# Performance work log

Hardware: AMD Instinct MI355X
Metric: run time of the kernel (lower is better)

## Reference

```python
import jax, jax.numpy as jnp
import numpy as np
from jax.scipy.linalg import solve_triangular

B, S, H, D, L = 8, 256, 768, 128, 64


def setup_inputs() -> dict:
    key = jax.random.key(0)
    ks = jax.random.split(key, 14)
    f = lambda k, shp, s=1.0: (jax.random.normal(k, shp, dtype=jnp.float32) * s)
    return {
        'word_feat_mean': f(ks[0], (B, S, H)),
        'word_feat_div': f(ks[1], (B, S, H)),
        'sent_feat_mean': f(ks[2], (B, 1, H)),
        'sent_feat_div': f(ks[3], (B, 1, H)),
        'W1': f(ks[4], (H, D), 0.02), 'b1': f(ks[5], (D,), 0.02),
        'W2': f(ks[6], (H, D), 0.02), 'b2': f(ks[7], (D,), 0.02),
        'W3': f(ks[8], (H, D), 0.02), 'b3': f(ks[9], (D,), 0.02),
        'W4': f(ks[10], (H, D), 0.02), 'b4': f(ks[11], (D,), 0.02),
        'label_mean': f(ks[12], (L, D)),
        'label_div_vec': f(ks[13], (L, D)),
    }


def _jsd_rank1(mu_p, v_p, mu_q, v_q):
    """Symmetric Gaussian JSD (0.5*(KL12+KL21)) between N(mu_p, I+v_p v_p^T) (labels, [L,D])
    and N(mu_q, I+v_q v_q^T) (words, [B,S,D]) via Sherman-Morrison closed form -> [B,L,S].
    Same math as torch.distributions MVN KL with Sigma = I + vv^T."""
    d = mu_p.shape[-1]
    n_p = 1.0 + jnp.sum(v_p * v_p, -1)            # [L]   = det(I+vp vp^T)
    n_q = 1.0 + jnp.sum(v_q * v_q, -1)            # [B,S]
    dot = jnp.einsum('ld,bsd->bls', v_p, v_q)     # vp.vq
    # ||mu_q - mu_p||^2 expanded without materializing [B,L,S,D]
    d2 = (jnp.sum(mu_q * mu_q, -1)[:, None, :]
          - 2.0 * jnp.einsum('ld,bsd->bls', mu_p, mu_q)
          + jnp.sum(mu_p * mu_p, -1)[None, :, None])
    vq_delta = (jnp.einsum('bsd,bsd->bs', v_q, mu_q)[:, None, :]
                - jnp.einsum('ld,bsd->bls', mu_p, v_q))
    vp_delta = (jnp.einsum('ld,bsd->bls', v_p, mu_q)
                - jnp.sum(v_p * mu_p, -1)[None, :, None])
    n_p_b = n_p[None, :, None]
    n_q_b = n_q[:, None, :]
    maha_q = d2 - vq_delta ** 2 / n_q_b           # delta^T Sigma_q^{-1} delta
    maha_p = d2 - vp_delta ** 2 / n_p_b
    tr_pq = d + (n_p_b - 1.0) - ((n_q_b - 1.0) + dot ** 2) / n_q_b  # tr(Sq^{-1} Sp)
    tr_qp = d + (n_q_b - 1.0) - ((n_p_b - 1.0) + dot ** 2) / n_p_b
    kl_pq = 0.5 * (jnp.log(n_q_b) - jnp.log(n_p_b) - d + tr_pq + maha_q)
    kl_qp = 0.5 * (jnp.log(n_p_b) - jnp.log(n_q_b) - d + tr_qp + maha_p)
    return 0.5 * (kl_pq + kl_qp)


def _jsd_full(mu_p, S_p, mu_q, S_q):
    """Symmetric JSD between full-covariance Gaussians, Cholesky-based (like torch MVN KL).
    mu_*: [..., D], S_*: [..., D, D] -> [...]."""
    d = mu_p.shape[-1]
    L_p = jnp.linalg.cholesky(S_p)
    L_q = jnp.linalg.cholesky(S_q)
    logdet_p = 2.0 * jnp.sum(jnp.log(jnp.diagonal(L_p, axis1=-2, axis2=-1)), -1)
    logdet_q = 2.0 * jnp.sum(jnp.log(jnp.diagonal(L_q, axis1=-2, axis2=-1)), -1)
    delta = mu_q - mu_p

    def kl(La, Lb, logda, logdb):
        # KL(a||b) = 0.5*(logdet_b - logdet_a - d + tr(Sb^{-1}Sa) + delta^T Sb^{-1} delta)
        X = solve_triangular(Lb, La, lower=True)
        tr = jnp.sum(X * X, axis=(-1, -2))
        y = solve_triangular(Lb, delta[..., None], lower=True)[..., 0]
        maha = jnp.sum(y * y, -1)
        return 0.5 * (logdb - logda - d + tr + maha)

    return 0.5 * (kl(L_p, L_q, logdet_p, logdet_q) + kl(L_q, L_p, logdet_q, logdet_p))


def reference(word_feat_mean, word_feat_div, sent_feat_mean, sent_feat_div,
              W1, b1, W2, b2, W3, b3, W4, b4, label_mean, label_div_vec):
    Bx, Sx, _ = word_feat_mean.shape
    Dx = W1.shape[1]
    Lx = label_mean.shape[0]
    wm = word_feat_mean @ W1 + b1        # jw1: [B,S,D]
    wv = word_feat_div @ W2 + b2         # jw2: [B,S,D]
    sm = sent_feat_mean @ W3 + b3        # jw3: [B,1,D]
    sv = sent_feat_div @ W4 + b4         # jw4: [B,1,D]
    eye = jnp.eye(Dx, dtype=wm.dtype)
    # Gaussian JSD attention: q = labels, k = v = words (closed-form, no [B,L*S,D,D])
    score = jax.nn.softmax(_jsd_rank1(label_mean, label_div_vec, wm, wv), axis=-1)  # [B,L,S]
    v_mean = jnp.einsum('bls,bsd->bld', score, wm)
    word_cov = eye + wv[..., :, None] * wv[..., None, :]                 # [B,S,D,D]
    v_div = jnp.einsum('bls,bsde->blde', score, word_cov)                # [B,L,D,D]
    sent_cov = eye + sv[..., :, None] * sv[..., None, :]                 # [B,1,D,D]
    text_mean = (sm + v_mean) / 2                                        # [B,L,D]
    text_div = (sent_cov + v_div) / 2                                    # [B,L,D,D]
    label_cov = eye + label_div_vec[:, :, None] * label_div_vec[:, None, :]  # [L,D,D]
    lm_b = jnp.broadcast_to(label_mean, (Bx, Lx, Dx))
    lc_b = jnp.broadcast_to(label_cov, (Bx, Lx, Dx, Dx))
    relate_score = _jsd_full(text_mean, text_div, lm_b, lc_b)            # [B,L]
    return relate_score, lm_b, lc_b
```

## Files before the change

kernel.cpp:

```cpp
#include <hip/hip_runtime.h>
#include <hip/hip_bf16.h>


#define PITCH 132

typedef __attribute__((ext_vector_type(8))) short bf16x8;
typedef __attribute__((ext_vector_type(4))) float f32x4;

__device__ __forceinline__ float bf2f(unsigned int u) {
    union { unsigned int i; float f; } c; c.i = u << 16; return c.f;
}
__device__ __forceinline__ unsigned short f2bf(float f) {
    __hip_bfloat16 h = __float2bfloat16(f);
    union { __hip_bfloat16 h; unsigned short u; } c; c.h = h; return c.u;
}

__global__ __launch_bounds__(256, 2)
void k1_gemm(const float* __restrict__ Am, const float* __restrict__ Av,
             const float* __restrict__ sfm, const float* __restrict__ sfd,
             const float* __restrict__ W1, const float* __restrict__ B1,
             const float* __restrict__ W2, const float* __restrict__ B2,
             const float* __restrict__ W3, const float* __restrict__ B3,
             const float* __restrict__ W4, const float* __restrict__ B4,
             float* __restrict__ wm, float* __restrict__ wv,
             float* __restrict__ sm, float* __restrict__ sv,
             unsigned short* __restrict__ wvTg) {
    __shared__ float At[16][64];
// ... 40 lines not shown
#pragma unroll
        for (int c = 0; c < 8; ++c) {
            float vl = acc[c] + Bs[j0 + c];
            D[ob + c] = vl;
            tileT[r][j0 + c] = vl;
        }
    }
    if (sel && !sentB) {
        __syncthreads();
        int d = tid >> 1, h = tid & 1;
        unsigned short u[8];
#pragma unroll
        for (int ss = 0; ss < 8; ++ss) u[ss] = f2bf(tileT[h * 8 + ss][d]);
        unsigned int p0 = (unsigned int)u[0] | ((unsigned int)u[1] << 16);
        unsigned int p1 = (unsigned int)u[2] | ((unsigned int)u[3] << 16);
        unsigned int p2 = (unsigned int)u[4] | ((unsigned int)u[5] << 16);
        unsigned int p3 = (unsigned int)u[6] | ((unsigned int)u[7] << 16);
        unsigned short* dst = wvTg + (size_t)(R0 >> 8) * 32768 + (size_t)d * 256 + (R0 & 255) + h * 8;
        *(uint4*)dst = make_uint4(p0, p1, p2, p3);
    }
}

template <int N>
__device__ __forceinline__ void bsumN(float* v, float* red) {
#pragma unroll
    for (int o = 32; o; o >>= 1)
#pragma unroll
        for (int n = 0; n < N; ++n) v[n] += __shfl_xor(v[n], o);
    __syncthreads();
    if ((threadIdx.x & 63) == 0) {
        int w = threadIdx.x >> 6;
#pragma unroll
        for (int n = 0; n < N; ++n) red[w * N + n] = v[n];
    }
    __syncthreads();
#pragma unroll
    for (int n = 0; n < N; ++n)
        v[n] = red[0 * N + n] + red[1 * N + n] + red[2 * N + n] + red[3 * N + n];
    __syncthreads();
}

__global__ __launch_bounds__(256, 2)
void k4_fused(const float* __restrict__ wm, const float* __restrict__ wv,
              const unsigned short* __restrict__ wvTg,
              const float* __restrict__ smg, const float* __restrict__ svg,
              const float* __restrict__ lmg, const float* __restrict__ ldvg,
              float* __restrict__ out) {
    extern __shared__ float smem[];
    float* Amat = smem;
    float* Wb   = smem + 16896;
    float* Sbuf = Wb;
    float* ssq  = smem + 19008;
    float* svr  = smem + 19264;
    float* vrow = smem + 19392;
    float* zv   = smem + 19520;
    float* zd   = smem + 19648;
    float* red  = smem + 19776;
    float* scoreL = Amat;
    float* vpart  = Amat + 256;

    const int tid = threadIdx.x;
    const int bid = blockIdx.x;
    const int b = bid >> 6, l = bid & 63;

    if (tid < 128) {
        svr[tid]  = svg[b * 128 + tid];
        vrow[tid] = ldvg[l * 128 + tid];
        zv[tid]   = lmg[l * 128 + tid];
    }
    __syncthreads();
    if (tid < 32) {
        float4 v = *(const float4*)&lmg[l * 128 + tid * 4];
        *(float4*)&out[512 + (size_t)bid * 128 + tid * 4] = v;
    }
    {
        float* lcb = out + 512 + 65536 + (size_t)bid * 16384;
#pragma unroll
        for (int q = 0; q < 16; ++q) {
            int flat4 = q * 256 + tid;
            int i = flat4 >> 5;
            int j4 = (flat4 & 31) * 4;
            float vi = vrow[i];
            float4 r;
            r.x = vi * vrow[j4 + 0] + ((i == j4 + 0) ? 1.f : 0.f);
            r.y = vi * vrow[j4 + 1] + ((i == j4 + 1) ? 1.f : 0.f);
            r.z = vi * vrow[j4 + 2] + ((i == j4 + 2) ? 1.f : 0.f);
            r.w = vi * vrow[j4 + 3] + ((i == j4 + 3) ? 1.f : 0.f);
            *(float4*)&lcb[(size_t)flat4 * 4] = r;
        }
    }
    float lv[3] = {0.f, 0.f, 0.f};
    if (tid < 128) {
        float m = zv[tid], v = vrow[tid];
        lv[0] = m * m; lv[1] = v * v; lv[2] = m * v;
    }
    bsumN<3>(lv, red);
    const float mmp = lv[0], np = 1.f + lv[1], vmp = lv[2];
    const float4* wmr = (const float4*)(wm + (size_t)(b * 256 + tid) * 128);
    const float4* wvr = (const float4*)(wv + (size_t)(b * 256 + tid) * 128);
    float md = 0.f, dot = 0.f, pvv = 0.f, vq = 0.f;
    float smm = 0.f, svv = 0.f, smv = 0.f;
#pragma unroll 8
    for (int q = 0; q < 32; ++q) {
        float4 xm = wmr[q], xv = wvr[q];
        const float* m4 = &zv[q * 4];
        const float* v4 = &vrow[q * 4];
        md  += m4[0] * xm.x + m4[1] * xm.y + m4[2] * xm.z + m4[3] * xm.w;
        dot += v4[0] * xv.x + v4[1] * xv.y + v4[2] * xv.z + v4[3] * xv.w;
        pvv += m4[0] * xv.x + m4[1] * xv.y + m4[2] * xv.z + m4[3] * xv.w;
        vq  += v4[0] * xm.x + v4[1] * xm.y + v4[2] * xm.z + v4[3] * xm.w;
        smm += xm.x * xm.x + xm.y * xm.y + xm.z * xm.z + xm.w * xm.w;
        svv += xv.x * xv.x + xv.y * xv.y + xv.z * xv.z + xv.w * xv.w;
        smv += xm.x * xv.x + xm.y * xv.y + xm.z * xv.z + xm.w * xv.w;
    }
    float nq = 1.f + svv;
    float d2 = smm - 2.f * md + mmp;
    float vqd = smv - pvv, vpd = vq - vmp;
    float inq = 1.f / nq, inp = 1.f / np;
    float maha_q = d2 - vqd * vqd * inq;
    float maha_p = d2 - vpd * vpd * inp;
    float logit = 0.25f * ((np - 1.f) + (nq - 1.f)
                           - (nq - 1.f + dot * dot) * inq
                           - (np - 1.f + dot * dot) * inp
                           + maha_q + maha_p);
    float mx = logit;
#pragma unroll
    for (int o = 32; o; o >>= 1) mx = fmaxf(mx, __shfl_xor(mx, o));
    if ((tid & 63) == 0) red[tid >> 6] = mx;
    __syncthreads();
    mx = fmaxf(fmaxf(red[0], red[1]), fmaxf(red[2], red[3]));
    float e = expf(logit - mx);
    float s = e;
#pragma unroll
    for (int o = 32; o; o >>= 1) s += __shfl_xor(s, o);
    __syncthreads();
    if ((tid & 63) == 0) red[tid >> 6] = s;
    __syncthreads();
    float tot = red[0] + red[1] + red[2] + red[3];
    float sc = e / tot;
    scoreL[tid] = sc;
    ssq[tid] = sqrtf(sc);
    __syncthreads();
    {
        int d4 = (tid & 31) * 4, sg = tid >> 5;
        const float* wmb = wm + (size_t)b * 256 * 128;
        float ax = 0.f, ay = 0.f, az = 0.f, aw = 0.f;
        for (int s2 = sg * 32; s2 < sg * 32 + 32; ++s2) {
            float w = scoreL[s2];
            float4 x = *(const float4*)&wmb[(size_t)s2 * 128 + d4];
            ax += w * x.x; ay += w * x.y; az += w * x.z; aw += w * x.w;
        }
        *(float4*)&vpart[sg * 128 + d4] = make_float4(ax, ay, az, aw);
    }
    __syncthreads();
    if (tid < 128) {
        float vm8 = 0.f;
#pragma unroll
        for (int g2 = 0; g2 < 8; ++g2) vm8 += vpart[g2 * 128 + tid];
        zd[tid] = zv[tid] - 0.5f * (smg[b * 128 + tid] + vm8);
        zv[tid] = vrow[tid];
    }
    __syncthreads();
    {
        unsigned short* Sb = (unsigned short*)Amat;
        const unsigned short* src = wvTg + (size_t)b * 32768;
        const int s0 = (tid & 31) * 8;
        float ssv[8];
#pragma unroll
        for (int j = 0; j < 8; ++j) ssv[j] = ssq[s0 + j];
#pragma unroll
        for (int it = 0; it < 16; ++it) {
            int f8 = tid + it * 256;
            int d = f8 >> 5;
            uint4 raw = *(const uint4*)&src[(size_t)f8 * 8];
            unsigned int p0 = (unsigned int)f2bf(bf2f(raw.x & 0xffffu) * ssv[0])
                            | ((unsigned int)f2bf(bf2f(raw.x >> 16) * ssv[1]) << 16);
            unsigned int p1 = (unsigned int)f2bf(bf2f(raw.y & 0xffffu) * ssv[2])
                            | ((unsigned int)f2bf(bf2f(raw.y >> 16) * ssv[3]) << 16);
            unsigned int p2 = (unsigned int)f2bf(bf2f(raw.z & 0xffffu) * ssv[4])
                            | ((unsigned int)f2bf(bf2f(raw.z >> 16) * ssv[5]) << 16);
            unsigned int p3 = (unsigned int)f2bf(bf2f(raw.w & 0xffffu) * ssv[6])
                            | ((unsigned int)f2bf(bf2f(raw.w >> 16) * ssv[7]) << 16);
            *(uint4*)&Sb[(size_t)d * 264 + s0] = make_uint4(p0, p1, p2, p3);
        }
    }
    __syncthreads();
    {
        const unsigned short* Sb = (const unsigned short*)Amat;
        const int w = tid >> 6, ln = tid & 63;
        const int rl = ln & 15, g = ln >> 4;
        const int arow0 = 16 * w + rl;
        const int arow1 = 16 * (w + 4) + rl;
        f32x4 acc0[8], acc1[8];
#pragma unroll
        for (int t = 0; t < 8; ++t) {
            acc0[t] = (f32x4){0.f, 0.f, 0.f, 0.f};
            acc1[t] = (f32x4){0.f, 0.f, 0.f, 0.f};
        }
#pragma unroll
        for (int ks = 0; ks < 8; ++ks) {
            bf16x8 a0 = *(const bf16x8*)&Sb[(size_t)arow0 * 264 + ks * 32 + g * 8];
            bf16x8 a1 = *(const bf16x8*)&Sb[(size_t)arow1 * 264 + ks * 32 + g * 8];
#pragma unroll
            for (int tj = 0; tj < 8; ++tj) {
                bf16x8 bb = *(const bf16x8*)&Sb[(size_t)(16 * tj + rl) * 264 + ks * 32 + g * 8];
                acc0[tj] = __builtin_amdgcn_mfma_f32_16x16x32_bf16(a0, bb, acc0[tj], 0, 0, 0);
                acc1[tj] = __builtin_amdgcn_mfma_f32_16x16x32_bf16(a1, bb, acc1[tj], 0, 0, 0);
            }
        }
        __syncthreads();
#pragma unroll
        for (int tj = 0; tj < 8; ++tj) {
            int j = 16 * tj + rl;
            float svj = svr[j];
#pragma unroll
            for (int r = 0; r < 4; ++r) {
                int i = 16 * w + g * 4 + r;
                Amat[i * PITCH + j] = ((i == j) ? 1.f : 0.f) + 0.5f * (svr[i] * svj + acc0[tj][r]);
                int i2 = 16 * (w + 4) + g * 4 + r;
                Amat[i2 * PITCH + j] = ((i2 == j) ? 1.f : 0.f) + 0.5f * (svr[i2] * svj + acc1[tj][r]);
            }
        }
    }
    __syncthreads();
    float v5[5] = {0.f, 0.f, 0.f, 0.f, 0.f};
    if (tid < 128) {
        v5[0] = Amat[tid * PITCH + tid];
        float vv = vrow[tid], de = zd[tid];
        v5[1] = vv * vv; v5[2] = de * de; v5[3] = vv * de;
    }
    {
        int i = tid >> 1, h = tid & 1;
        const float* Ar = &Amat[i * PITCH + h * 64];
        const float* vr = &vrow[h * 64];
        float s2 = 0.f;
        for (int k2 = 0; k2 < 64; k2 += 4) {
            float4 a = *(const float4*)&Ar[k2];
            s2 += a.x * vr[k2] + a.y * vr[k2 + 1] + a.z * vr[k2 + 2] + a.w * vr[k2 + 3];
        }
        v5[4] = vrow[i] * s2;
    }
    bsumN<5>(v5, red);
    const float trP = v5[0], nv = v5[1], dds = v5[2], vds = v5[3], vsv = v5[4];
    for (int p = 0; p < 8; ++p) {
        const int base = 16 * p;
        const int R = 112 - base;
        __syncthreads();
        if (p > 0) {
            const int pb = base - 16;
            if (tid >= base && tid < 128) {
                int i = tid;
                const float* Lr = &Amat[i * PITCH + pb];
                float dv = 0.f, dd2 = 0.f;
#pragma unroll
                for (int t = 0; t < 16; ++t) {
                    float lvv = Lr[t];
                    dv  += lvv * zv[pb + t];
                    dd2 += lvv * zd[pb + t];
                }
                zv[i] -= dv; zd[i] -= dd2;
            }
            int njobs = (R + 16) * 16;
            for (int idx = tid; idx < njobs; idx += 256) {
                int r2 = idx >> 4, jc = idx & 15;
                int i = base + r2, j = base + jc;
                if (j <= i) {
                    const float* wi = &Wb[i];
                    const float* wj = &Wb[j];
                    float acc2 = 0.f;
#pragma unroll
                    for (int t = 0; t < 16; ++t)
                        acc2 += wi[t * PITCH] * wj[t * PITCH];
                    Amat[i * PITCH + j] -= acc2;
                }
            }
        }
        __syncthreads();
        if (tid < 64) {
            const int c = tid;
            float cv[16];
            if (c < 16) {
#pragma unroll
                for (int r2 = 0; r2 < 16; ++r2) {
                    int hi = (r2 >= c) ? r2 : c, lo2 = (r2 >= c) ? c : r2;
                    cv[r2] = Amat[(base + hi) * PITCH + base + lo2];
                }
            } else {
#pragma unroll
                for (int r2 = 0; r2 < 16; ++r2) cv[r2] = 0.f;
            }
#pragma unroll
            for (int t = 0; t < 16; ++t) {
                float lt[16];
#pragma unroll
                for (int r2 = 0; r2 < 16; ++r2) lt[r2] = __shfl(cv[r2], t);
                float invs = 1.f / sqrtf(lt[t]);
                if (c == t) {
#pragma unroll
                    for (int r2 = 0; r2 < 16; ++r2) cv[r2] = (r2 >= t) ? lt[r2] * invs : 0.f;
                } else if (c > t && c < 16) {
                    float lc = lt[c] * invs;
#pragma unroll
                    for (int r2 = 0; r2 < 16; ++r2)
                        if (r2 > t) cv[r2] -= (lt[r2] * invs) * lc;
                }
            }
            float x[16], acb[16];
#pragma unroll
            for (int r2 = 0; r2 < 16; ++r2) acb[r2] = 0.f;
#pragma unroll
            for (int r2 = 0; r2 < 16; ++r2) {
                float Lrr = __shfl(cv[r2], r2);
                float xr = (((c == r2) ? 1.f : 0.f) - acb[r2]) / Lrr;
                x[r2] = xr;
#pragma unroll
                for (int q = r2 + 1; q < 16; ++q) acb[q] += __shfl(cv[q], r2) * xr;
            }
            if (c < 16) {
#pragma unroll
                for (int r2 = 0; r2 < 16; ++r2)
                    Amat[(base + c) * PITCH + base + r2] = x[r2];
            }
            if (c < 32) {
                int t2 = c & 15;
                float* zp = (c < 16) ? zv : zd;
                float a0 = 0.f;
#pragma unroll
                for (int a = 0; a < 16; ++a)
                    a0 += Amat[(base + a) * PITCH + base + t2] * zp[base + a];
                zp[base + t2] = a0;
            }
        } else if (p > 0 && R > 0) {
            int nt = R >> 3;
            int ntri = (nt * (nt + 1)) >> 1;
            for (int tau = tid - 64; tau < ntri; tau += 192) {
                float ft = sqrtf(8.f * (float)tau + 1.f);
                int tr = (int)((ft - 1.f) * 0.5f);
                while (((tr + 1) * (tr + 2)) / 2 <= tau) ++tr;
                while ((tr * (tr + 1)) / 2 > tau) --tr;
                int tc = tau - ((tr * (tr + 1)) >> 1);
                int ii = base + 16 + tr * 8, jj = base + 16 + tc * 8;
                float a2[8][8];
#pragma unroll
                for (int r2 = 0; r2 < 8; ++r2)
#pragma unroll
                    for (int c2 = 0; c2 < 8; ++c2) a2[r2][c2] = 0.f;
#pragma unroll
                for (int t = 0; t < 16; ++t) {
                    const float* wr = &Wb[t * PITCH];
                    float4 x0 = *(const float4*)&wr[ii];
                    float4 x1 = *(const float4*)&wr[ii + 4];
                    float4 y0 = *(const float4*)&wr[jj];
                    float4 y1 = *(const float4*)&wr[jj + 4];
                    float xa[8] = {x0.x,x0.y,x0.z,x0.w, x1.x,x1.y,x1.z,x1.w};
                    float yb[8] = {y0.x,y0.y,y0.z,y0.w, y1.x,y1.y,y1.z,y1.w};
#pragma unroll
                    for (int r2 = 0; r2 < 8; ++r2)
#pragma unroll
                        for (int c2 = 0; c2 < 8; ++c2) a2[r2][c2] += xa[r2] * yb[c2];
                }
#pragma unroll
                for (int r2 = 0; r2 < 8; ++r2) {
                    float* Ar2 = &Amat[(ii + r2) * PITCH + jj];
                    float4 u0 = *(float4*)&Ar2[0];
                    float4 u1 = *(float4*)&Ar2[4];
                    u0.x -= a2[r2][0]; u0.y -= a2[r2][1]; u0.z -= a2[r2][2]; u0.w -= a2[r2][3];
                    u1.x -= a2[r2][4]; u1.y -= a2[r2][5]; u1.z -= a2[r2][6]; u1.w -= a2[r2][7];
                    *(float4*)&Ar2[0] = u0;
                    *(float4*)&Ar2[4] = u1;
                }
            }
        }
        __syncthreads();
        if (R > 0 && tid < R) {
            int i = base + 16 + tid;
            const float* Ar = &Amat[i * PITCH + base];
            float4 q0 = *(const float4*)&Ar[0];
            float4 q1 = *(const float4*)&Ar[4];
            float4 q2 = *(const float4*)&Ar[8];
            float4 q3 = *(const float4*)&Ar[12];
            float rA[16] = {q0.x,q0.y,q0.z,q0.w, q1.x,q1.y,q1.z,q1.w,
                            q2.x,q2.y,q2.z,q2.w, q3.x,q3.y,q3.z,q3.w};
            float lo[16];
#pragma unroll
            for (int t = 0; t < 16; ++t) lo[t] = 0.f;
#pragma unroll
            for (int a = 0; a < 16; ++a) {
                float va = rA[a];
                const float* Trow = &Amat[(base + a) * PITCH + base];
                float4 t0 = *(const float4*)&Trow[0];
                float4 t1 = *(const float4*)&Trow[4];
                float4 t2 = *(const float4*)&Trow[8];
                float4 t3 = *(const float4*)&Trow[12];
                lo[0] += va * t0.x; lo[1] += va * t0.y; lo[2] += va * t0.z; lo[3] += va * t0.w;
                lo[4] += va * t1.x; lo[5] += va * t1.y; lo[6] += va * t1.z; lo[7] += va * t1.w;
                lo[8] += va * t2.x; lo[9] += va * t2.y; lo[10] += va * t2.z; lo[11] += va * t2.w;
                lo[12] += va * t3.x; lo[13] += va * t3.y; lo[14] += va * t3.z; lo[15] += va * t3.w;
            }
            float* Aw = &Amat[i * PITCH + base];
            *(float4*)&Aw[0]  = make_float4(lo[0], lo[1], lo[2], lo[3]);
            *(float4*)&Aw[4]  = make_float4(lo[4], lo[5], lo[6], lo[7]);
            *(float4*)&Aw[8]  = make_float4(lo[8], lo[9], lo[10], lo[11]);
            *(float4*)&Aw[12] = make_float4(lo[12], lo[13], lo[14], lo[15]);
#pragma unroll
            for (int t = 0; t < 16; ++t) Wb[t * PITCH + i] = lo[t];
        }
    }
    for (int s2 = 1; s2 <= 7; ++s2) {
        __syncthreads();
        int npair = 8 - s2;
        int jobs = npair * 16;
        int len = 16 * s2;
        for (int t = tid; t < jobs; t += 256) {
            int pr = t >> 4;
            int ta = (t >> 2) & 3, tb = t & 3;
            int i = pr + s2, J = pr;
            const float* u0 = &Amat[(16 * i + ta * 4) * PITCH + 16 * J];
            const float* w0 = &Amat[(16 * J + tb * 4) * PITCH + 16 * J];
            float a4[4][4];
#pragma unroll
            for (int r2 = 0; r2 < 4; ++r2)
#pragma unroll
                for (int c2 = 0; c2 < 4; ++c2) a4[r2][c2] = 0.f;
            for (int k = 0; k < len; k += 4) {
                float4 ur[4], wr4[4];
#pragma unroll
                for (int r2 = 0; r2 < 4; ++r2) ur[r2] = *(const float4*)&u0[r2 * PITCH + k];
#pragma unroll
                for (int c2 = 0; c2 < 4; ++c2) wr4[c2] = *(const float4*)&w0[c2 * PITCH + k];
#pragma unroll
                for (int r2 = 0; r2 < 4; ++r2)
#pragma unroll
                    for (int c2 = 0; c2 < 4; ++c2)
                        a4[r2][c2] += ur[r2].x * wr4[c2].x + ur[r2].y * wr4[c2].y
                                    + ur[r2].z * wr4[c2].z + ur[r2].w * wr4[c2].w;
            }
#pragma unroll
            for (int r2 = 0; r2 < 4; ++r2)
#pragma unroll
                for (int c2 = 0; c2 < 4; ++c2)
                    Sbuf[pr * 256 + (ta * 4 + r2) * 16 + tb * 4 + c2] = a4[r2][c2];
        }
        __syncthreads();
        for (int idx = tid; idx < npair * 256; idx += 256) {
            int pr = idx >> 8;
            int J = pr, i = pr + s2;
            int cc = (idx >> 4) & 15, bb = idx & 15;
            float a0 = 0.f;
#pragma unroll
            for (int a = 0; a < 16; ++a)
                a0 += Amat[(16 * i + a) * PITCH + 16 * i + cc] * Sbuf[pr * 256 + a * 16 + bb];
            Amat[(16 * J + bb) * PITCH + 16 * i + cc] = -a0;
        }
    }
    __syncthreads();
    float v3[3] = {0.f, 0.f, 0.f};
    {
        int i = tid & 127, h = tid >> 7;
        int c0 = (i >> 4) << 4;
        int half = (128 - c0) >> 1;
        const float* Ar = &Amat[i * PITCH + c0 + h * half];
        for (int k2 = 0; k2 < half; k2 += 4) {
            float4 a = *(const float4*)&Ar[k2];
            v3[0] += a.x * a.x + a.y * a.y + a.z * a.z + a.w * a.w;
        }
    }
    if (tid < 128) {
        float a = zv[tid];  v3[1] = a * a;
        float d22 = zd[tid]; v3[2] = d22 * d22;
    }
    bsumN<3>(v3, red);
    if (tid == 0) {
        float n = 1.f + nv;
        float Aterm = trP - vsv / n;
        float Bt = v3[0] + v3[1];
        float mq = dds - vds * vds / n;
        out[bid] = 0.25f * (Aterm + Bt - 256.f + mq + v3[2]);
    }
}

extern "C" void kernel_launch(void* const* d_in, const int* in_sizes, int n_in,
                              void* d_out, int out_size, void* d_ws, size_t ws_size,
                              hipStream_t stream) {
    const float* wfm = (const float*)d_in[0];
    const float* wfd = (const float*)d_in[1];
    const float* sfm = (const float*)d_in[2];
    const float* sfd = (const float*)d_in[3];
    const float* W1 = (const float*)d_in[4];
    const float* B1 = (const float*)d_in[5];
    const float* W2 = (const float*)d_in[6];
    const float* B2 = (const float*)d_in[7];
    const float* W3 = (const float*)d_in[8];
    const float* B3 = (const float*)d_in[9];
    const float* W4 = (const float*)d_in[10];
    const float* B4 = (const float*)d_in[11];
    const float* lm = (const float*)d_in[12];
    const float* ldv = (const float*)d_in[13];
    float* out = (float*)d_out;
    float* ws = (float*)d_ws;

    float* wm = ws;
    float* wv = ws + 262144;
    float* sm = ws + 524288;
    float* sv = ws + 525312;
    unsigned short* wvTg = (unsigned short*)(ws + 731392);

    constexpr int SH_FLOATS = 19800;
    constexpr size_t SH_BYTES = SH_FLOATS * sizeof(float);
    (void)hipFuncSetAttribute((const void*)k4_fused,
                              hipFuncAttributeMaxDynamicSharedMemorySize,
                              (int)SH_BYTES);

    k1_gemm<<<dim3(129, 2), 256, 0, stream>>>(wfm, wfd, sfm, sfd,
                                              W1, B1, W2, B2, W3, B3, W4, B4,
                                              wm, wv, sm, sv, wvTg);
    k4_fused<<<512, 256, SH_BYTES, stream>>>(wm, wv, wvTg, sm, sv, lm, ldv, out);
}
```

Baseline: 212.2 us.

## Process two labels per block to share word-feature loads and halve grid

Each k4_fused block now handles two labels for the same batch instead of one. The wm/wv rows, the scaled wvT tile source and the reductions are shared across both labels, and the triangular-solve stages are interleaved across two Amat/Wb buffers. The aim is to halve redundant global reads of word features and improve per-thread work in the latency-bound solve phases. In exchange, LDS use roughly doubles to about 158KB, which lowers occupancy, and the grid shrinks to 256 blocks, which reduces parallelism across CUs.

Result: slower. 219.6 us (+3.5%).

```diff
diff --git a/kernel.cpp b/kernel.cpp
--- a/kernel.cpp
+++ b/kernel.cpp
@@ -3,6 +3,18 @@
 
 
 #define PITCH 132
+#define AM0   0
+#define AM1   16896
+#define WB0   33792
+#define WB1   35904
+#define SSQ   38016
+#define SVR   38528
+#define VR    38656
+#define ZV    38912
+#define ZD    39168
+#define LABS  39424
+#define RED   39432
+#define SH_FLOATS 39464
 
 typedef __attribute__((ext_vector_type(8))) short bf16x8;
 typedef __attribute__((ext_vector_type(4))) float f32x4;
@@ -89,7 +101,7 @@
 }
 
 template <int N>
-__device__ __forceinline__ void bsumN(float* v, float* red) {
+__device__ __forceinline__ void bsum2(float* v, float* red) {
 #pragma unroll
     for (int o = 32; o; o >>= 1)
 #pragma unroll
@@ -101,9 +113,10 @@
         for (int n = 0; n < N; ++n) red[w * N + n] = v[n];
     }
     __syncthreads();
+    int h = threadIdx.x >> 7;
 #pragma unroll
     for (int n = 0; n < N; ++n)
-        v[n] = red[0 * N + n] + red[1 * N + n] + red[2 * N + n] + red[3 * N + n];
+        v[n] = red[(2 * h) * N + n] + red[(2 * h + 1) * N + n];
     __syncthreads();
 }
 
@@ -114,243 +127,308 @@
               const float* __restrict__ lmg, const float* __restrict__ ldvg,
               float* __restrict__ out) {
     extern __shared__ float smem[];
-    float* Amat = smem;
-    float* Wb   = smem + 16896;
-    float* Sbuf = Wb;
-    float* ssq  = smem + 19008;
-    float* svr  = smem + 19264;
-    float* vrow = smem + 19392;
-    float* zv   = smem + 19520;
-    float* zd   = smem + 19648;
-    float* red  = smem + 19776;
-    float* scoreL = Amat;
-    float* vpart  = Amat + 256;
+    float* red  = smem + RED;
+    float* labs = smem + LABS;
 
     const int tid = threadIdx.x;
     const int bid = blockIdx.x;
-    const int b = bid >> 6, l = bid & 63;
+    const int b = bid >> 5;
+    const int l0 = (bid & 31) * 2;
 
     if (tid < 128) {
-        svr[tid]  = svg[b * 128 + tid];
-        vrow[tid] = ldvg[l * 128 + tid];
-        zv[tid]   = lmg[l * 128 + tid];
-    }
-    __syncthreads();
-    if (tid < 32) {
-        float4 v = *(const float4*)&lmg[l * 128 + tid * 4];
-        *(float4*)&out[512 + (size_t)bid * 128 + tid * 4] = v;
-    }
-    {
-        float* lcb = out + 512 + 65536 + (size_t)bid * 16384;
+        smem[SVR + tid] = svg[b * 128 + tid];
+        smem[VR + tid]        = ldvg[(size_t)l0 * 128 + tid];
+        smem[VR + 128 + tid]  = ldvg[(size_t)(l0 + 1) * 128 + tid];
+        smem[ZV + tid]        = lmg[(size_t)l0 * 128 + tid];
+        smem[ZV + 128 + tid]  = lmg[(size_t)(l0 + 1) * 128 + tid];
+    }
+    __syncthreads();
+#pragma unroll
+    for (int p2 = 0; p2 < 2; ++p2) {
+        const int l_ = l0 + p2;
+        const float* vr = smem + VR + p2 * 128;
+        if (tid < 32) {
+            float4 v = *(const float4*)&lmg[(size_t)l_ * 128 + tid * 4];
+            *(float4*)&out[512 + (size_t)(b * 64 + l_) * 128 + tid * 4] = v;
+        }
+        float* lcb = out + 512 + 65536 + (size_t)(b * 64 + l_) * 16384;
 #pragma unroll
         for (int q = 0; q < 16; ++q) {
             int flat4 = q * 256 + tid;
             int i = flat4 >> 5;
             int j4 = (flat4 & 31) * 4;
-            float vi = vrow[i];
+            float vi = vr[i];
             float4 r;
-            r.x = vi * vrow[j4 + 0] + ((i == j4 + 0) ? 1.f : 0.f);
-            r.y = vi * vrow[j4 + 1] + ((i == j4 + 1) ? 1.f : 0.f);
-            r.z = vi * vrow[j4 + 2] + ((i == j4 + 2) ? 1.f : 0.f);
-            r.w = vi * vrow[j4 + 3] + ((i == j4 + 3) ? 1.f : 0.f);
+            r.x = vi * vr[j4 + 0] + ((i == j4 + 0) ? 1.f : 0.f);
+            r.y = vi * vr[j4 + 1] + ((i == j4 + 1) ? 1.f : 0.f);
+            r.z = vi * vr[j4 + 2] + ((i == j4 + 2) ? 1.f : 0.f);
+            r.w = vi * vr[j4 + 3] + ((i == j4 + 3) ? 1.f : 0.f);
             *(float4*)&lcb[(size_t)flat4 * 4] = r;
         }
     }
-    float lv[3] = {0.f, 0.f, 0.f};
-    if (tid < 128) {
-        float m = zv[tid], v = vrow[tid];
+    {
+        float lv[3] = {0.f, 0.f, 0.f};
+        int t = tid & 127, h = tid >> 7;
+        float m = smem[ZV + h * 128 + t], v = smem[VR + h * 128 + t];
         lv[0] = m * m; lv[1] = v * v; lv[2] = m * v;
-    }
-    bsumN<3>(lv, red);
-    const float mmp = lv[0], np = 1.f + lv[1], vmp = lv[2];
-    const float4* wmr = (const float4*)(wm + (size_t)(b * 256 + tid) * 128);
-    const float4* wvr = (const float4*)(wv + (size_t)(b * 256 + tid) * 128);
-    float md = 0.f, dot = 0.f, pvv = 0.f, vq = 0.f;
-    float smm = 0.f, svv = 0.f, smv = 0.f;
-#pragma unroll 8
-    for (int q = 0; q < 32; ++q) {
-        float4 xm = wmr[q], xv = wvr[q];
-        const float* m4 = &zv[q * 4];
-        const float* v4 = &vrow[q * 4];
-        md  += m4[0] * xm.x + m4[1] * xm.y + m4[2] * xm.z + m4[3] * xm.w;
-        dot += v4[0] * xv.x + v4[1] * xv.y + v4[2] * xv.z + v4[3] * xv.w;
-        pvv += m4[0] * xv.x + m4[1] * xv.y + m4[2] * xv.z + m4[3] * xv.w;
-        vq  += v4[0] * xm.x + v4[1] * xm.y + v4[2] * xm.z + v4[3] * xm.w;
-        smm += xm.x * xm.x + xm.y * xm.y + xm.z * xm.z + xm.w * xm.w;
-        svv += xv.x * xv.x + xv.y * xv.y + xv.z * xv.z + xv.w * xv.w;
-        smv += xm.x * xv.x + xm.y * xv.y + xm.z * xv.z + xm.w * xv.w;
-    }
-    float nq = 1.f + svv;
-    float d2 = smm - 2.f * md + mmp;
-    float vqd = smv - pvv, vpd = vq - vmp;
-    float inq = 1.f / nq, inp = 1.f / np;
-    float maha_q = d2 - vqd * vqd * inq;
-    float maha_p = d2 - vpd * vpd * inp;
-    float logit = 0.25f * ((np - 1.f) + (nq - 1.f)
-                           - (nq - 1.f + dot * dot) * inq
-                           - (np - 1.f + dot * dot) * inp
-                           + maha_q + maha_p);
-    float mx = logit;
-#pragma unroll
-    for (int o = 32; o; o >>= 1) mx = fmaxf(mx, __shfl_xor(mx, o));
-    if ((tid & 63) == 0) red[tid >> 6] = mx;
-    __syncthreads();
-    mx = fmaxf(fmaxf(red[0], red[1]), fmaxf(red[2], red[3]));
-    float e = expf(logit - mx);
-    float s = e;
-#pragma unroll
-    for (int o = 32; o; o >>= 1) s += __shfl_xor(s, o);
-    __syncthreads();
-    if ((tid & 63) == 0) red[tid >> 6] = s;
-    __syncthreads();
-    float tot = red[0] + red[1] + red[2] + red[3];
-    float sc = e / tot;
-    scoreL[tid] = sc;
-    ssq[tid] = sqrtf(sc);
+        bsum2<3>(lv, red);
+        if ((tid & 127) == 0) {
+            int hh = tid >> 7;
+            labs[hh * 3 + 0] = lv[0]; labs[hh * 3 + 1] = lv[1]; labs[hh * 3 + 2] = lv[2];
+        }
+    }
+    __syncthreads();
+    const float mmp0 = labs[0], np0 = 1.f + labs[1], vmp0 = labs[2];
+    const float mmp1 = labs[3], np1 = 1.f + labs[4], vmp1 = labs[5];
+    float logit0, logit1;
+    {
+        const float4* wmr = (const float4*)(wm + (size_t)(b * 256 + tid) * 128);
+        const float4* wvr = (const float4*)(wv + (size_t)(b * 256 + tid) * 128);
+        const float* mu0 = smem + ZV;       const float* mu1 = smem + ZV + 128;
+        const float* vp0 = smem + VR;       const float* vp1 = smem + VR + 128;
+        float md0 = 0.f, md1 = 0.f, dot0 = 0.f, dot1 = 0.f;
+        float pv0 = 0.f, pv1 = 0.f, vq0 = 0.f, vq1 = 0.f;
+        float smm = 0.f, svv = 0.f, smv = 0.f;
+#pragma unroll 4
+        for (int q = 0; q < 32; ++q) {
+            float4 xm = wmr[q], xv = wvr[q];
+            const float* m0 = &mu0[q * 4]; const float* m1 = &mu1[q * 4];
+            const float* v0 = &vp0[q * 4]; const float* v1 = &vp1[q * 4];
+            md0 += m0[0]*xm.x + m0[1]*xm.y + m0[2]*xm.z + m0[3]*xm.w;
+            md1 += m1[0]*xm.x + m1[1]*xm.y + m1[2]*xm.z + m1[3]*xm.w;
+            dot0 += v0[0]*xv.x + v0[1]*xv.y + v0[2]*xv.z + v0[3]*xv.w;
+            dot1 += v1[0]*xv.x + v1[1]*xv.y + v1[2]*xv.z + v1[3]*xv.w;
+            pv0 += m0[0]*xv.x + m0[1]*xv.y + m0[2]*xv.z + m0[3]*xv.w;
+            pv1 += m1[0]*xv.x + m1[1]*xv.y + m1[2]*xv.z + m1[3]*xv.w;
+            vq0 += v0[0]*xm.x + v0[1]*xm.y + v0[2]*xm.z + v0[3]*xm.w;
+            vq1 += v1[0]*xm.x + v1[1]*xm.y + v1[2]*xm.z + v1[3]*xm.w;
+            smm += xm.x*xm.x + xm.y*xm.y + xm.z*xm.z + xm.w*xm.w;
+            svv += xv.x*xv.x + xv.y*xv.y + xv.z*xv.z + xv.w*xv.w;
+            smv += xm.x*xv.x + xm.y*xv.y + xm.z*xv.z + xm.w*xv.w;
+        }
+        float nq = 1.f + svv, inq = 1.f / nq;
+        {
+            float d2 = smm - 2.f * md0 + mmp0;
+            float vqd = smv - pv0, vpd = vq0 - vmp0;
+            float inp = 1.f / np0;
+            float mq = d2 - vqd * vqd * inq;
+            float mp = d2 - vpd * vpd * inp;
+            logit0 = 0.25f * ((np0 - 1.f) + (nq - 1.f)
+                              - (nq - 1.f + dot0 * dot0) * inq
+                              - (np0 - 1.f + dot0 * dot0) * inp + mq + mp);
+        }
+        {
+            float d2 = smm - 2.f * md1 + mmp1;
+            float vqd = smv - pv1, vpd = vq1 - vmp1;
+            float inp = 1.f / np1;
+            float mq = d2 - vqd * vqd * inq;
+            float mp = d2 - vpd * vpd * inp;
+            logit1 = 0.25f * ((np1 - 1.f) + (nq - 1.f)
+                              - (nq - 1.f + dot1 * dot1) * inq
+                              - (np1 - 1.f + dot1 * dot1) * inp + mq + mp);
+        }
+    }
+    {
+        float m0 = logit0, m1 = logit1;
+#pragma unroll
+        for (int o = 32; o; o >>= 1) {
+            m0 = fmaxf(m0, __shfl_xor(m0, o));
+            m1 = fmaxf(m1, __shfl_xor(m1, o));
+        }
+        if ((tid & 63) == 0) { red[tid >> 6] = m0; red[4 + (tid >> 6)] = m1; }
+        __syncthreads();
+        float mx0 = fmaxf(fmaxf(red[0], red[1]), fmaxf(red[2], red[3]));
+        float mx1 = fmaxf(fmaxf(red[4], red[5]), fmaxf(red[6], red[7]));
+        float e0 = expf(logit0 - mx0), e1 = expf(logit1 - mx1);
+        float s0 = e0, s1 = e1;
+#pragma unroll
+        for (int o = 32; o; o >>= 1) { s0 += __shfl_xor(s0, o); s1 += __shfl_xor(s1, o); }
+        __syncthreads();
+        if ((tid & 63) == 0) { red[tid >> 6] = s0; red[4 + (tid >> 6)] = s1; }
+        __syncthreads();
+        float tot0 = red[0] + red[1] + red[2] + red[3];
+        float tot1 = red[4] + red[5] + red[6] + red[7];
+        float sc0 = e0 / tot0, sc1 = e1 / tot1;
+        smem[AM0 + tid] = sc0;
+        smem[AM1 + tid] = sc1;
+        smem[SSQ + tid] = sqrtf(sc0);
+        smem[SSQ + 256 + tid] = sqrtf(sc1);
+    }
     __syncthreads();
     {
         int d4 = (tid & 31) * 4, sg = tid >> 5;
         const float* wmb = wm + (size_t)b * 256 * 128;
-        float ax = 0.f, ay = 0.f, az = 0.f, aw = 0.f;
+        const float* sc0 = smem + AM0;
+        const float* sc1 = smem + AM1;
+        float a0x=0.f,a0y=0.f,a0z=0.f,a0w=0.f, a1x=0.f,a1y=0.f,a1z=0.f,a1w=0.f;
         for (int s2 = sg * 32; s2 < sg * 32 + 32; ++s2) {
-            float w = scoreL[s2];
+            float w0 = sc0[s2], w1 = sc1[s2];
             float4 x = *(const float4*)&wmb[(size_t)s2 * 128 + d4];
-            ax += w * x.x; ay += w * x.y; az += w * x.z; aw += w * x.w;
-        }
-        *(float4*)&vpart[sg * 128 + d4] = make_float4(ax, ay, az, aw);
-    }
-    __syncthreads();
-    if (tid < 128) {
-        float vm8 = 0.f;
-#pragma unroll
-        for (int g2 = 0; g2 < 8; ++g2) vm8 += vpart[g2 * 128 + tid];
-        zd[tid] = zv[tid] - 0.5f * (smg[b * 128 + tid] + vm8);
-        zv[tid] = vrow[tid];
-    }
-    __syncthreads();
-    {
-        unsigned short* Sb = (unsigned short*)Amat;
+            a0x += w0 * x.x; a0y += w0 * x.y; a0z += w0 * x.z; a0w += w0 * x.w;
+            a1x += w1 * x.x; a1y += w1 * x.y; a1z += w1 * x.z; a1w += w1 * x.w;
+        }
+        *(float4*)&smem[AM0 + 256 + sg * 128 + d4] = make_float4(a0x, a0y, a0z, a0w);
+        *(float4*)&smem[AM1 + 256 + sg * 128 + d4] = make_float4(a1x, a1y, a1z, a1w);
+    }
+    __syncthreads();
+    {
+        int t = tid & 127, h = tid >> 7;
+        const float* vp = smem + ((h == 0) ? AM0 : AM1) + 256;
+        float vm = 0.f;
+#pragma unroll
+        for (int g2 = 0; g2 < 8; ++g2) vm += vp[g2 * 128 + t];
+        smem[ZD + h * 128 + t] = smem[ZV + h * 128 + t]
+                               - 0.5f * (smg[b * 128 + t] + vm);
+        smem[ZV + h * 128 + t] = smem[VR + h * 128 + t];
+    }
+    __syncthreads();
+    {
+        unsigned short* Sb0 = (unsigned short*)(smem + AM0);
+        unsigned short* Sb1 = (unsigned short*)(smem + AM1);
         const unsigned short* src = wvTg + (size_t)b * 32768;
         const int s0 = (tid & 31) * 8;
-        float ssv[8];
-#pragma unroll
-        for (int j = 0; j < 8; ++j) ssv[j] = ssq[s0 + j];
+        float sv0[8], sv1[8];
+#pragma unroll
+        for (int j = 0; j < 8; ++j) {
+            sv0[j] = smem[SSQ + s0 + j];
+            sv1[j] = smem[SSQ + 256 + s0 + j];
+        }
 #pragma unroll
         for (int it = 0; it < 16; ++it) {
             int f8 = tid + it * 256;
             int d = f8 >> 5;
             uint4 raw = *(const uint4*)&src[(size_t)f8 * 8];
-            unsigned int p0 = (unsigned int)f2bf(bf2f(raw.x & 0xffffu) * ssv[0])
-                            | ((unsigned int)f2bf(bf2f(raw.x >> 16) * ssv[1]) << 16);
-            unsigned int p1 = (unsigned int)f2bf(bf2f(raw.y & 0xffffu) * ssv[2])
-                            | ((unsigned int)f2bf(bf2f(raw.y >> 16) * ssv[3]) << 16);
-            unsigned int p2 = (unsigned int)f2bf(bf2f(raw.z & 0xffffu) * ssv[4])
-                            | ((unsigned int)f2bf(bf2f(raw.z >> 16) * ssv[5]) << 16);
-            unsigned int p3 = (unsigned int)f2bf(bf2f(raw.w & 0xffffu) * ssv[6])
-                            | ((unsigned int)f2bf(bf2f(raw.w >> 16) * ssv[7]) << 16);
-            *(uint4*)&Sb[(size_t)d * 264 + s0] = make_uint4(p0, p1, p2, p3);
-        }
-    }
-    __syncthreads();
-    {
-        const unsigned short* Sb = (const unsigned short*)Amat;
+            float f[8] = { bf2f(raw.x & 0xffffu), bf2f(raw.x >> 16),
+                           bf2f(raw.y & 0xffffu), bf2f(raw.y >> 16),
+                           bf2f(raw.z & 0xffffu), bf2f(raw.z >> 16),
+                           bf2f(raw.w & 0xffffu), bf2f(raw.w >> 16) };
+            uint4 o0, o1;
+            o0.x = (unsigned int)f2bf(f[0]*sv0[0]) | ((unsigned int)f2bf(f[1]*sv0[1]) << 16);
+            o0.y = (unsigned int)f2bf(f[2]*sv0[2]) | ((unsigned int)f2bf(f[3]*sv0[3]) << 16);
+            o0.z = (unsigned int)f2bf(f[4]*sv0[4]) | ((unsigned int)f2bf(f[5]*sv0[5]) << 16);
+            o0.w = (unsigned int)f2bf(f[6]*sv0[6]) | ((unsigned int)f2bf(f[7]*sv0[7]) << 16);
+            o1.x = (unsigned int)f2bf(f[0]*sv1[0]) | ((unsigned int)f2bf(f[1]*sv1[1]) << 16);
+            o1.y = (unsigned int)f2bf(f[2]*sv1[2]) | ((unsigned int)f2bf(f[3]*sv1[3]) << 16);
+            o1.z = (unsigned int)f2bf(f[4]*sv1[4]) | ((unsigned int)f2bf(f[5]*sv1[5]) << 16);
+            o1.w = (unsigned int)f2bf(f[6]*sv1[6]) | ((unsigned int)f2bf(f[7]*sv1[7]) << 16);
+            *(uint4*)&Sb0[(size_t)d * 264 + s0] = o0;
+            *(uint4*)&Sb1[(size_t)d * 264 + s0] = o1;
+        }
+    }
+    __syncthreads();
+    {
         const int w = tid >> 6, ln = tid & 63;
         const int rl = ln & 15, g = ln >> 4;
-        const int arow0 = 16 * w + rl;
-        const int arow1 = 16 * (w + 4) + rl;
-        f32x4 acc0[8], acc1[8];
-#pragma unroll
-        for (int t = 0; t < 8; ++t) {
-            acc0[t] = (f32x4){0.f, 0.f, 0.f, 0.f};
-            acc1[t] = (f32x4){0.f, 0.f, 0.f, 0.f};
-        }
-#pragma unroll
-        for (int ks = 0; ks < 8; ++ks) {
-            bf16x8 a0 = *(const bf16x8*)&Sb[(size_t)arow0 * 264 + ks * 32 + g * 8];
-            bf16x8 a1 = *(const bf16x8*)&Sb[(size_t)arow1 * 264 + ks * 32 + g * 8];
+#pragma unroll
+        for (int p2 = 0; p2 < 2; ++p2) {
+            const unsigned short* Sb = (const unsigned short*)(smem + (p2 ? AM1 : AM0));
+            float* Am = smem + (p2 ? AM1 : AM0);
+            const int arow0 = 16 * w + rl;
+            const int arow1 = 16 * (w + 4) + rl;
+            f32x4 acc0[8], acc1[8];
+#pragma unroll
+            for (int t = 0; t < 8; ++t) {
+                acc0[t] = (f32x4){0.f, 0.f, 0.f, 0.f};
+                acc1[t] = (f32x4){0.f, 0.f, 0.f, 0.f};
+            }
+#pragma unroll
+            for (int ks = 0; ks < 8; ++ks) {
+                bf16x8 a0 = *(const bf16x8*)&Sb[(size_t)arow0 * 264 + ks * 32 + g * 8];
+                bf16x8 a1 = *(const bf16x8*)&Sb[(size_t)arow1 * 264 + ks * 32 + g * 8];
+#pragma unroll
+                for (int tj = 0; tj < 8; ++tj) {
+                    bf16x8 bb = *(const bf16x8*)&Sb[(size_t)(16 * tj + rl) * 264 + ks * 32 + g * 8];
+                    acc0[tj] = __builtin_amdgcn_mfma_f32_16x16x32_bf16(a0, bb, acc0[tj], 0, 0, 0);
+                    acc1[tj] = __builtin_amdgcn_mfma_f32_16x16x32_bf16(a1, bb, acc1[tj], 0, 0, 0);
+                }
+            }
+            __syncthreads();
 #pragma unroll
             for (int tj = 0; tj < 8; ++tj) {
-                bf16x8 bb = *(const bf16x8*)&Sb[(size_t)(16 * tj + rl) * 264 + ks * 32 + g * 8];
-                acc0[tj] = __builtin_amdgcn_mfma_f32_16x16x32_bf16(a0, bb, acc0[tj], 0, 0, 0);
-                acc1[tj] = __builtin_amdgcn_mfma_f32_16x16x32_bf16(a1, bb, acc1[tj], 0, 0, 0);
-            }
-        }
-        __syncthreads();
-#pragma unroll
-        for (int tj = 0; tj < 8; ++tj) {
-            int j = 16 * tj + rl;
-            float svj = svr[j];
-#pragma unroll
-            for (int r = 0; r < 4; ++r) {
-                int i = 16 * w + g * 4 + r;
-                Amat[i * PITCH + j] = ((i == j) ? 1.f : 0.f) + 0.5f * (svr[i] * svj + acc0[tj][r]);
-                int i2 = 16 * (w + 4) + g * 4 + r;
-                Amat[i2 * PITCH + j] = ((i2 == j) ? 1.f : 0.f) + 0.5f * (svr[i2] * svj + acc1[tj][r]);
-            }
-        }
-    }
-    __syncthreads();
-    float v5[5] = {0.f, 0.f, 0.f, 0.f, 0.f};
-    if (tid < 128) {
-        v5[0] = Amat[tid * PITCH + tid];
-        float vv = vrow[tid], de = zd[tid];
+                int j = 16 * tj + rl;
+                float svj = smem[SVR + j];
+#pragma unroll
+                for (int r = 0; r < 4; ++r) {
+                    int i = 16 * w + g * 4 + r;
+                    Am[i * PITCH + j] = ((i == j) ? 1.f : 0.f)
+                                      + 0.5f * (smem[SVR + i] * svj + acc0[tj][r]);
+                    int i2 = 16 * (w + 4) + g * 4 + r;
+                    Am[i2 * PITCH + j] = ((i2 == j) ? 1.f : 0.f)
+                                       + 0.5f * (smem[SVR + i2] * svj + acc1[tj][r]);
+                }
+            }
+        }
+    }
+    __syncthreads();
+    float trP, nv, dds, vds, vsv;
+    {
+        float v5[5] = {0.f, 0.f, 0.f, 0.f, 0.f};
+        int t = tid & 127, h = tid >> 7;
+        const float* Am = smem + (h ? AM1 : AM0);
+        const float* vr = smem + VR + h * 128;
+        v5[0] = Am[t * PITCH + t];
+        float vv = vr[t], de = smem[ZD + h * 128 + t];
         v5[1] = vv * vv; v5[2] = de * de; v5[3] = vv * de;
-    }
-    {
-        int i = tid >> 1, h = tid & 1;
-        const float* Ar = &Amat[i * PITCH + h * 64];
-        const float* vr = &vrow[h * 64];
+        const float* Ar = &Am[t * PITCH];
         float s2 = 0.f;
-        for (int k2 = 0; k2 < 64; k2 += 4) {
+        for (int k2 = 0; k2 < 128; k2 += 4) {
             float4 a = *(const float4*)&Ar[k2];
             s2 += a.x * vr[k2] + a.y * vr[k2 + 1] + a.z * vr[k2 + 2] + a.w * vr[k2 + 3];
         }
-        v5[4] = vrow[i] * s2;
-    }
-    bsumN<5>(v5, red);
-    const float trP = v5[0], nv = v5[1], dds = v5[2], vds = v5[3], vsv = v5[4];
+        v5[4] = vv * s2;
+        bsum2<5>(v5, red);
+        trP = v5[0]; nv = v5[1]; dds = v5[2]; vds = v5[3]; vsv = v5[4];
+    }
     for (int p = 0; p < 8; ++p) {
         const int base = 16 * p;
         const int R = 112 - base;
         __syncthreads();
         if (p > 0) {
             const int pb = base - 16;
-            if (tid >= base && tid < 128) {
-                int i = tid;
-                const float* Lr = &Amat[i * PITCH + pb];
+            int t = tid & 127, h = tid >> 7;
+            float* Am = smem + (h ? AM1 : AM0);
+            float* Wbh = smem + (h ? WB1 : WB0);
+            float* zvh = smem + ZV + h * 128;
+            float* zdh = smem + ZD + h * 128;
+            if (t >= base) {
+                int i = t;
+                const float* Lr = &Am[i * PITCH + pb];
                 float dv = 0.f, dd2 = 0.f;
 #pragma unroll
-                for (int t = 0; t < 16; ++t) {
-                    float lvv = Lr[t];
-                    dv  += lvv * zv[pb + t];
-                    dd2 += lvv * zd[pb + t];
-                }
-                zv[i] -= dv; zd[i] -= dd2;
+                for (int t2 = 0; t2 < 16; ++t2) {
+                    float lvv = Lr[t2];
+                    dv  += lvv * zvh[pb + t2];
+                    dd2 += lvv * zdh[pb + t2];
+                }
+                zvh[i] -= dv; zdh[i] -= dd2;
             }
             int njobs = (R + 16) * 16;
-            for (int idx = tid; idx < njobs; idx += 256) {
+            for (int idx = t; idx < njobs; idx += 128) {
                 int r2 = idx >> 4, jc = idx & 15;
                 int i = base + r2, j = base + jc;
                 if (j <= i) {
-                    const float* wi = &Wb[i];
-                    const float* wj = &Wb[j];
+                    const float* wi = &Wbh[i];
+                    const float* wj = &Wbh[j];
                     float acc2 = 0.f;
 #pragma unroll
-                    for (int t = 0; t < 16; ++t)
-                        acc2 += wi[t * PITCH] * wj[t * PITCH];
-                    Amat[i * PITCH + j] -= acc2;
-                }
-            }
-        }
-        __syncthreads();
-        if (tid < 64) {
-            const int c = tid;
+                    for (int t2 = 0; t2 < 16; ++t2)
+                        acc2 += wi[t2 * PITCH] * wj[t2 * PITCH];
+                    Am[i * PITCH + j] -= acc2;
+                }
+            }
+        }
+        __syncthreads();
+        if (tid < 128) {
+            const int h = tid >> 6, c = tid & 63;
+            float* Am = smem + (h ? AM1 : AM0);
+            float* zvh = smem + ZV + h * 128;
+            float* zdh = smem + ZD + h * 128;
             float cv[16];
             if (c < 16) {
 #pragma unroll
                 for (int r2 = 0; r2 < 16; ++r2) {
                     int hi = (r2 >= c) ? r2 : c, lo2 = (r2 >= c) ? c : r2;
-                    cv[r2] = Amat[(base + hi) * PITCH + base + lo2];
+                    cv[r2] = Am[(base + hi) * PITCH + base + lo2];
                 }
             } else {
 #pragma unroll
@@ -386,21 +464,25 @@
             if (c < 16) {
 #pragma unroll
                 for (int r2 = 0; r2 < 16; ++r2)
-                    Amat[(base + c) * PITCH + base + r2] = x[r2];
+                    Am[(base + c) * PITCH + base + r2] = x[r2];
             }
             if (c < 32) {
                 int t2 = c & 15;
-                float* zp = (c < 16) ? zv : zd;
+                float* zp = (c < 16) ? zvh : zdh;
                 float a0 = 0.f;
 #pragma unroll
                 for (int a = 0; a < 16; ++a)
-                    a0 += Amat[(base + a) * PITCH + base + t2] * zp[base + a];
+                    a0 += Am[(base + a) * PITCH + base + t2] * zp[base + a];
                 zp[base + t2] = a0;
             }
         } else if (p > 0 && R > 0) {
             int nt = R >> 3;
             int ntri = (nt * (nt + 1)) >> 1;
-            for (int tau = tid - 64; tau < ntri; tau += 192) {
+            for (int tau2 = tid - 128; tau2 < 2 * ntri; tau2 += 128) {
+                int h2 = (tau2 >= ntri) ? 1 : 0;
+                int tau = tau2 - h2 * ntri;
+                float* Am = smem + (h2 ? AM1 : AM0);
+                float* Wbh = smem + (h2 ? WB1 : WB0);
                 float ft = sqrtf(8.f * (float)tau + 1.f);
                 int tr = (int)((ft - 1.f) * 0.5f);
                 while (((tr + 1) * (tr + 2)) / 2 <= tau) ++tr;
@@ -414,7 +496,7 @@
                     for (int c2 = 0; c2 < 8; ++c2) a2[r2][c2] = 0.f;
 #pragma unroll
                 for (int t = 0; t < 16; ++t) {
-                    const float* wr = &Wb[t * PITCH];
+                    const float* wr = &Wbh[t * PITCH];
                     float4 x0 = *(const float4*)&wr[ii];
                     float4 x1 = *(const float4*)&wr[ii + 4];
                     float4 y0 = *(const float4*)&wr[jj];
@@ -428,7 +510,7 @@
                 }
 #pragma unroll
                 for (int r2 = 0; r2 < 8; ++r2) {
-                    float* Ar2 = &Amat[(ii + r2) * PITCH + jj];
+                    float* Ar2 = &Am[(ii + r2) * PITCH + jj];
                     float4 u0 = *(float4*)&Ar2[0];
                     float4 u1 = *(float4*)&Ar2[4];
                     u0.x -= a2[r2][0]; u0.y -= a2[r2][1]; u0.z -= a2[r2][2]; u0.w -= a2[r2][3];
@@ -439,38 +521,43 @@
             }
         }
         __syncthreads();
-        if (R > 0 && tid < R) {
-            int i = base + 16 + tid;
-            const float* Ar = &Amat[i * PITCH + base];
-            float4 q0 = *(const float4*)&Ar[0];
-            float4 q1 = *(const float4*)&Ar[4];
-            float4 q2 = *(const float4*)&Ar[8];
-            float4 q3 = *(const float4*)&Ar[12];
-            float rA[16] = {q0.x,q0.y,q0.z,q0.w, q1.x,q1.y,q1.z,q1.w,
-                            q2.x,q2.y,q2.z,q2.w, q3.x,q3.y,q3.z,q3.w};
-            float lo[16];
-#pragma unroll
-            for (int t = 0; t < 16; ++t) lo[t] = 0.f;
-#pragma unroll
-            for (int a = 0; a < 16; ++a) {
-                float va = rA[a];
-                const float* Trow = &Amat[(base + a) * PITCH + base];
-                float4 t0 = *(const float4*)&Trow[0];
-                float4 t1 = *(const float4*)&Trow[4];
-                float4 t2 = *(const float4*)&Trow[8];
-                float4 t3 = *(const float4*)&Trow[12];
-                lo[0] += va * t0.x; lo[1] += va * t0.y; lo[2] += va * t0.z; lo[3] += va * t0.w;
-                lo[4] += va * t1.x; lo[5] += va * t1.y; lo[6] += va * t1.z; lo[7] += va * t1.w;
-                lo[8] += va * t2.x; lo[9] += va * t2.y; lo[10] += va * t2.z; lo[11] += va * t2.w;
-                lo[12] += va * t3.x; lo[13] += va * t3.y; lo[14] += va * t3.z; lo[15] += va * t3.w;
-            }
-            float* Aw = &Amat[i * PITCH + base];
-            *(float4*)&Aw[0]  = make_float4(lo[0], lo[1], lo[2], lo[3]);
-            *(float4*)&Aw[4]  = make_float4(lo[4], lo[5], lo[6], lo[7]);
-            *(float4*)&Aw[8]  = make_float4(lo[8], lo[9], lo[10], lo[11]);
-            *(float4*)&Aw[12] = make_float4(lo[12], lo[13], lo[14], lo[15]);
-#pragma unroll
-            for (int t = 0; t < 16; ++t) Wb[t * PITCH + i] = lo[t];
+        if (R > 0) {
+            int t = tid & 127, h = tid >> 7;
+            if (t < R) {
+                float* Am = smem + (h ? AM1 : AM0);
+                float* Wbh = smem + (h ? WB1 : WB0);
+                int i = base + 16 + t;
+                const float* Ar = &Am[i * PITCH + base];
+                float4 q0 = *(const float4*)&Ar[0];
+                float4 q1 = *(const float4*)&Ar[4];
+                float4 q2 = *(const float4*)&Ar[8];
+                float4 q3 = *(const float4*)&Ar[12];
+                float rA[16] = {q0.x,q0.y,q0.z,q0.w, q1.x,q1.y,q1.z,q1.w,
+                                q2.x,q2.y,q2.z,q2.w, q3.x,q3.y,q3.z,q3.w};
+                float lo[16];
+#pragma unroll
+                for (int t2 = 0; t2 < 16; ++t2) lo[t2] = 0.f;
+#pragma unroll
+                for (int a = 0; a < 16; ++a) {
+                    float va = rA[a];
+                    const float* Trow = &Am[(base + a) * PITCH + base];
+                    float4 t0 = *(const float4*)&Trow[0];
+                    float4 t1 = *(const float4*)&Trow[4];
+                    float4 t2v = *(const float4*)&Trow[8];
+                    float4 t3 = *(const float4*)&Trow[12];
+                    lo[0] += va * t0.x; lo[1] += va * t0.y; lo[2] += va * t0.z; lo[3] += va * t0.w;
+                    lo[4] += va * t1.x; lo[5] += va * t1.y; lo[6] += va * t1.z; lo[7] += va * t1.w;
+                    lo[8] += va * t2v.x; lo[9] += va * t2v.y; lo[10] += va * t2v.z; lo[11] += va * t2v.w;
+                    lo[12] += va * t3.x; lo[13] += va * t3.y; lo[14] += va * t3.z; lo[15] += va * t3.w;
+                }
+                float* Aw = &Am[i * PITCH + base];
+                *(float4*)&Aw[0]  = make_float4(lo[0], lo[1], lo[2], lo[3]);
+                *(float4*)&Aw[4]  = make_float4(lo[4], lo[5], lo[6], lo[7]);
+                *(float4*)&Aw[8]  = make_float4(lo[8], lo[9], lo[10], lo[11]);
+                *(float4*)&Aw[12] = make_float4(lo[12], lo[13], lo[14], lo[15]);
+#pragma unroll
+                for (int t2 = 0; t2 < 16; ++t2) Wbh[t2 * PITCH + i] = lo[t2];
+            }
         }
     }
     for (int s2 = 1; s2 <= 7; ++s2) {
@@ -478,12 +565,16 @@
         int npair = 8 - s2;
         int jobs = npair * 16;
         int len = 16 * s2;
-        for (int t = tid; t < jobs; t += 256) {
-            int pr = t >> 4;
-            int ta = (t >> 2) & 3, tb = t & 3;
+        for (int t = tid; t < 2 * jobs; t += 256) {
+            int h2 = (t >= jobs) ? 1 : 0;
+            int tt = t - h2 * jobs;
+            float* Am = smem + (h2 ? AM1 : AM0);
+            float* Sb = smem + (h2 ? WB1 : WB0);
+            int pr = tt >> 4;
+            int ta = (tt >> 2) & 3, tb = tt & 3;
             int i = pr + s2, J = pr;
-            const float* u0 = &Amat[(16 * i + ta * 4) * PITCH + 16 * J];
-            const float* w0 = &Amat[(16 * J + tb * 4) * PITCH + 16 * J];
+            const float* u0 = &Am[(16 * i + ta * 4) * PITCH + 16 * J];
+            const float* w0 = &Am[(16 * J + tb * 4) * PITCH + 16 * J];
             float a4[4][4];
 #pragma unroll
             for (int r2 = 0; r2 < 4; ++r2)
@@ -506,43 +597,46 @@
             for (int r2 = 0; r2 < 4; ++r2)
 #pragma unroll
                 for (int c2 = 0; c2 < 4; ++c2)
-                    Sbuf[pr * 256 + (ta * 4 + r2) * 16 + tb * 4 + c2] = a4[r2][c2];
-        }
-        __syncthreads();
-        for (int idx = tid; idx < npair * 256; idx += 256) {
-            int pr = idx >> 8;
+                    Sb[pr * 256 + (ta * 4 + r2) * 16 + tb * 4 + c2] = a4[r2][c2];
+        }
+        __syncthreads();
+        int tot2 = npair * 256;
+        for (int idx = tid; idx < 2 * tot2; idx += 256) {
+            int h2 = (idx >= tot2) ? 1 : 0;
+            int ii2 = idx - h2 * tot2;
+            float* Am = smem + (h2 ? AM1 : AM0);
+            float* Sb = smem + (h2 ? WB1 : WB0);
+            int pr = ii2 >> 8;
             int J = pr, i = pr + s2;
-            int cc = (idx >> 4) & 15, bb = idx & 15;
+            int cc = (ii2 >> 4) & 15, bb = ii2 & 15;
             float a0 = 0.f;
 #pragma unroll
             for (int a = 0; a < 16; ++a)
-                a0 += Amat[(16 * i + a) * PITCH + 16 * i + cc] * Sbuf[pr * 256 + a * 16 + bb];
-            Amat[(16 * J + bb) * PITCH + 16 * i + cc] = -a0;
-        }
-    }
-    __syncthreads();
-    float v3[3] = {0.f, 0.f, 0.f};
-    {
-        int i = tid & 127, h = tid >> 7;
-        int c0 = (i >> 4) << 4;
-        int half = (128 - c0) >> 1;
-        const float* Ar = &Amat[i * PITCH + c0 + h * half];
-        for (int k2 = 0; k2 < half; k2 += 4) {
+                a0 += Am[(16 * i + a) * PITCH + 16 * i + cc] * Sb[pr * 256 + a * 16 + bb];
+            Am[(16 * J + bb) * PITCH + 16 * i + cc] = -a0;
+        }
+    }
+    __syncthreads();
+    {
+        float v3[3] = {0.f, 0.f, 0.f};
+        int t = tid & 127, h = tid >> 7;
+        const float* Am = smem + (h ? AM1 : AM0);
+        int c0 = (t >> 4) << 4;
+        const float* Ar = &Am[t * PITCH];
+        for (int k2 = c0; k2 < 128; k2 += 4) {
             float4 a = *(const float4*)&Ar[k2];
             v3[0] += a.x * a.x + a.y * a.y + a.z * a.z + a.w * a.w;
         }
-    }
-    if (tid < 128) {
-        float a = zv[tid];  v3[1] = a * a;
-        float d22 = zd[tid]; v3[2] = d22 * d22;
-    }
-    bsumN<3>(v3, red);
-    if (tid == 0) {
-        float n = 1.f + nv;
-        float Aterm = trP - vsv / n;
-        float Bt = v3[0] + v3[1];
-        float mq = dds - vds * vds / n;
-        out[bid] = 0.25f * (Aterm + Bt - 256.f + mq + v3[2]);
+        float a = smem[ZV + h * 128 + t];  v3[1] = a * a;
+        float d22 = smem[ZD + h * 128 + t]; v3[2] = d22 * d22;
+        bsum2<3>(v3, red);
+        if ((tid & 127) == 0) {
+            float n = 1.f + nv;
+            float Aterm = trP - vsv / n;
+            float Bt = v3[0] + v3[1];
+            float mq = dds - vds * vds / n;
+            out[b * 64 + l0 + h] = 0.25f * (Aterm + Bt - 256.f + mq + v3[2]);
+        }
     }
 }
 
@@ -572,8 +666,7 @@
     float* sv = ws + 525312;
     unsigned short* wvTg = (unsigned short*)(ws + 731392);
 
-    constexpr int SH_FLOATS = 19800;
-    constexpr size_t SH_BYTES = SH_FLOATS * sizeof(float);
+    constexpr size_t SH_BYTES = (size_t)SH_FLOATS * sizeof(float);
     (void)hipFuncSetAttribute((const void*)k4_fused,
                               hipFuncAttributeMaxDynamicSharedMemorySize,
                               (int)SH_BYTES);
@@ -581,5 +674,5 @@
     k1_gemm<<<dim3(129, 2), 256, 0, stream>>>(wfm, wfd, sfm, sfd,
                                               W1, B1, W2, B2, W3, B3, W4, B4,
                                               wm, wv, sm, sv, wvTg);
-    k4_fused<<<512, 256, SH_BYTES, stream>>>(wm, wv, wvTg, sm, sv, lm, ldv, out);
+    k4_fused<<<256, 256, SH_BYTES, stream>>>(wm, wv, wvTg, sm, sv, lm, ldv, out);
 }
```
